# Kernel optimization log

Hardware: AMD Instinct MI355X
Metric: run time of the kernel (lower is better)

Reference implementation:

```python
import jax, jax.numpy as jnp
import numpy as np

COMMITMENT_COST = 0.25


def setup_inputs() -> dict:
    key = jax.random.key(0)
    k1, k2 = jax.random.split(key)
    z = jax.random.normal(k1, (32, 256, 32, 32), dtype=jnp.float32)
    # codebook init matches torch uniform_(-1/codebook_size, 1/codebook_size)
    embedding = jax.random.uniform(k2, (1024, 256), dtype=jnp.float32,
                                   minval=-1.0 / 1024, maxval=1.0 / 1024)
    return {"z": z, "embedding": embedding}


def reference(z, embedding):
    # z: [B, C, H, W] -> [B, H, W, C]
    z_bhwc = jnp.transpose(z.astype(jnp.float32), (0, 2, 3, 1))
    B, H, W, C = z_bhwc.shape
    z_flat = z_bhwc.reshape(-1, C)                      # [N, C]

    # squared-distance matrix via norms + matmul: [N, K]
    d = (jnp.sum(z_flat ** 2, axis=1, keepdims=True)
         + jnp.sum(embedding ** 2, axis=1)
         - 2.0 * jnp.einsum('nc,kc->nk', z_flat, embedding))

    min_encoding_indices = jnp.argmin(d, axis=1)        # [N]
    z_quantized = embedding[min_encoding_indices].reshape(B, H, W, C)

    commitment_loss = COMMITMENT_COST * (jax.lax.stop_gradient(z_quantized) - z_bhwc) ** 2
    codebook_loss = (z_quantized - jax.lax.stop_gradient(z_bhwc)) ** 2
    loss = commitment_loss + codebook_loss              # [B, H, W, C]

    # straight-through estimator
    z_quantized = z_bhwc + jax.lax.stop_gradient(z_quantized - z_bhwc)
    z_quantized = jnp.transpose(z_quantized, (0, 3, 1, 2))  # [B, C, H, W]
    return z_quantized, loss, min_encoding_indices
```

## Files before the change

### kernel.cpp

```cpp
#include <hip/hip_runtime.h>

#define ZC     256
#define KCODES 1024
#define MARGIN 4e-4f
#define WIN    1e-4f
#define NPT    32768

typedef __attribute__((ext_vector_type(4))) float f32x4;
typedef __attribute__((ext_vector_type(8))) short s16x8;
typedef unsigned int u32t;
typedef u32t __attribute__((address_space(1))) as1_u32;
typedef u32t __attribute__((address_space(3))) as3_u32;

__device__ __forceinline__ void glds16(const void* g, void* l) {
    __builtin_amdgcn_global_load_lds((const as1_u32*)g, (as3_u32*)l, 16, 0, 0);
}
__device__ __forceinline__ unsigned short bf16_rn(float x) {
    union { float f; u32t u; } v; v.f = x;
    return (unsigned short)((v.u + 0x7FFFu + ((v.u >> 16) & 1u)) >> 16);
}

__global__ __launch_bounds__(256)
void vq_prep_z(const float* __restrict__ z, unsigned short* __restrict__ Ab)
{
    const int t = threadIdx.x, blk = blockIdx.x;
    const int pt = (blk >> 3) * 64 + (t & 63);
    const int c0 = (blk & 7) * 32 + (t >> 6) * 8;
    const int b = pt >> 10, hw = pt & 1023;
    const float* zp = z + (size_t)b * (ZC * 1024) + (size_t)c0 * 1024 + hw;

    unsigned short hi[8];
    #pragma unroll
    for (int j = 0; j < 8; ++j) hi[j] = bf16_rn(zp[(size_t)j * 1024]);
    uint4 ph;
    ph.x = (u32t)hi[0] | ((u32t)hi[1] << 16); ph.y = (u32t)hi[2] | ((u32t)hi[3] << 16);
    ph.z = (u32t)hi[4] | ((u32t)hi[5] << 16); ph.w = (u32t)hi[6] | ((u32t)hi[7] << 16);

    const size_t kb = (size_t)(c0 >> 6);
    const int sw = (c0 & 63) ^ ((pt & 7) << 3);
    *reinterpret_cast<uint4*>(Ab + kb * (32768ull * 64) + (size_t)pt * 64 + sw) = ph;
}

__global__ __launch_bounds__(256)
void vq_prep_e(const float* __restrict__ emb, unsigned short* __restrict__ Bb)
{
    const int t = threadIdx.x, blk = blockIdx.x;
    const int code = (blk >> 3) * 64 + (t & 63);
    const int c0 = (blk & 7) * 32 + (t >> 6) * 8;
    const float* ep = emb + (size_t)code * ZC + c0;

    unsigned short hi[8];
    #pragma unroll
    for (int j = 0; j < 8; ++j) hi[j] = bf16_rn(ep[j]);
    uint4 ph;
    ph.x = (u32t)hi[0] | ((u32t)hi[1] << 16); ph.y = (u32t)hi[2] | ((u32t)hi[3] << 16);
    ph.z = (u32t)hi[4] | ((u32t)hi[5] << 16); ph.w = (u32t)hi[6] | ((u32t)hi[7] << 16);

    const size_t kb = (size_t)(c0 >> 6);
    const int sw = (c0 & 63) ^ ((code & 7) << 3);
    *reinterpret_cast<uint4*>(Bb + kb * (1024ull * 64) + (size_t)code * 64 + sw) = ph;
}

__global__ __launch_bounds__(256)
void vq_ens_np(const float* __restrict__ emb, float* __restrict__ ens_np,
               int* __restrict__ cnt)
{
    if (blockIdx.x == 0 && threadIdx.x == 0) *cnt = 0;
    const int t = threadIdx.x, g = t >> 3, r = t & 7;
    const int code = blockIdx.x * 32 + g;
    const float* er = emb + (size_t)code * ZC;

    float lo, hi;
    {
        const float a0 = er[r], a1 = er[128 + r];
        lo = __fmul_rn(a0, a0); hi = __fmul_rn(a1, a1);
    }
    #pragma unroll
    for (int i = 1; i < 16; ++i) {
        const int c = 8 * i + r;
        const float a0 = er[c], a1 = er[128 + c];
        lo = __fadd_rn(lo, __fmul_rn(a0, a0));
        hi = __fadd_rn(hi, __fmul_rn(a1, a1));
    }
    #pragma unroll
    for (int mk = 1; mk < 8; mk <<= 1) {
        lo = __fadd_rn(lo, __shfl_xor(lo, mk));
        hi = __fadd_rn(hi, __shfl_xor(hi, mk));
    }
    if (r == 0) ens_np[code] = __fadd_rn(lo, hi);
}

__global__ __launch_bounds__(256, 2)
void vq_gemm_argmin(const unsigned short* __restrict__ Ab,
                    const unsigned short* __restrict__ Bb,
                    const float* __restrict__ ens_g,
                    float* __restrict__ partV1, float* __restrict__ partV2,
                    int* __restrict__ partI)
{
    __shared__ unsigned short As[64 * 64];
    __shared__ unsigned short Bs[128 * 64];

    const int t = threadIdx.x;
    const int lane = t & 63, wv = t >> 6;
    const int col = lane & 15, kg = lane >> 4;
    const int blk = blockIdx.x;
    const int pt0 = (blk >> 1) * 64;
    const int half = blk & 1;
    const int kx = (col & 7) << 3;

    int aoff[4][2], boff[2][2];
    #pragma unroll
    for (int m = 0; m < 4; ++m)
        #pragma unroll
        for (int s = 0; s < 2; ++s)
            aoff[m][s] = (m * 16 + col) * 64 + ((s * 32 + kg * 8) ^ kx);
    #pragma unroll
    for (int n = 0; n < 2; ++n)
        #pragma unroll
        for (int s = 0; s < 2; ++s)
            boff[n][s] = (wv * 32 + n * 16 + col) * 64 + ((s * 32 + kg * 8) ^ kx);

    f32x4 acc[4][2];
    #pragma unroll
    for (int m = 0; m < 4; ++m)
        #pragma unroll
        for (int n = 0; n < 2; ++n) acc[m][n] = (f32x4){0.f, 0.f, 0.f, 0.f};

    float v1[16], v2[16]; int id1[16];
    #pragma unroll
    for (int i = 0; i < 16; ++i) { v1[i] = 3.4e38f; v2[i] = 3.4e38f; id1[i] = 0; }

    for (int ci = 0; ci < 4; ++ci) {
        const int ct = half * 4 + ci;
        for (int ks = 0; ks < 4; ++ks) {
            const char* aS = (const char*)(Ab + (size_t)ks * 2097152ull + (size_t)pt0 * 64);
            const char* bS = (const char*)(Bb + (size_t)ks * 65536ull + (size_t)ct * 8192);

            __syncthreads();
            glds16(aS + t * 16,        (char*)As + t * 16);
            glds16(aS + 4096 + t * 16, (char*)As + 4096 + t * 16);
            #pragma unroll
            for (int q = 0; q < 4; ++q)
                glds16(bS + q * 4096 + t * 16, (char*)Bs + q * 4096 + t * 16);
            __syncthreads();

            s16x8 af[4][2], bf[2][2];
            #pragma unroll
            for (int m = 0; m < 4; ++m)
                #pragma unroll
                for (int s = 0; s < 2; ++s)
                    af[m][s] = *reinterpret_cast<const s16x8*>(As + aoff[m][s]);
            #pragma unroll
            for (int n = 0; n < 2; ++n)
                #pragma unroll
                for (int s = 0; s < 2; ++s)
                    bf[n][s] = *reinterpret_cast<const s16x8*>(Bs + boff[n][s]);
            #pragma unroll
            for (int m = 0; m < 4; ++m)
                #pragma unroll
                for (int n = 0; n < 2; ++n) {
                    acc[m][n] = __builtin_amdgcn_mfma_f32_16x16x32_bf16(af[m][0], bf[n][0], acc[m][n], 0, 0, 0);
                    acc[m][n] = __builtin_amdgcn_mfma_f32_16x16x32_bf16(af[m][1], bf[n][1], acc[m][n], 0, 0, 0);
                }

            if (ks == 3) {
                #pragma unroll
                for (int n = 0; n < 2; ++n) {
                    const int code = ct * 128 + wv * 32 + n * 16 + col;
                    const float en = ens_g[code];
                    #pragma unroll
                    for (int m = 0; m < 4; ++m)
                        #pragma unroll
                        for (int j = 0; j < 4; ++j) {
                            const float sc = fmaf(-2.f, acc[m][n][j], en);
                            const int sl = m * 4 + j;
                            if (sc < v1[sl]) { v2[sl] = v1[sl]; v1[sl] = sc; id1[sl] = code; }
                            else if (sc < v2[sl]) { v2[sl] = sc; }
                            acc[m][n][j] = 0.f;
                        }
                }
            }
        }
    }

    float w1[16], w2[16]; int wid[16];
    #pragma unroll
    for (int sl = 0; sl < 16; ++sl) {
        float a1 = v1[sl]; int ai = id1[sl]; float a2 = v2[sl];
        #pragma unroll
        for (int mk = 1; mk < 16; mk <<= 1) {
            const float o1 = __shfl_xor(a1, mk);
            const int   oi = __shfl_xor(ai, mk);
            const float o2 = __shfl_xor(a2, mk);
            if (o1 < a1)      { a2 = fminf(a1, o2); a1 = o1; ai = oi; }
            else if (o1 > a1) { a2 = fminf(a2, o1); }
            else              { a2 = (oi != ai) ? a1 : fminf(a2, o2); ai = (oi < ai) ? oi : ai; }
        }
        w1[sl] = a1; w2[sl] = a2; wid[sl] = ai;
    }

    __syncthreads();
    float* mv1 = reinterpret_cast<float*>(As);
    float* mv2 = mv1 + 256;
    int*   mid = reinterpret_cast<int*>(mv2 + 256);
    if (col == 0) {
        #pragma unroll
        for (int sl = 0; sl < 16; ++sl) {
            const int m = sl >> 2, j = sl & 3;
            const int p = m * 16 + kg * 4 + j;
            mv1[wv * 64 + p] = w1[sl];
            mv2[wv * 64 + p] = w2[sl];
            mid[wv * 64 + p] = wid[sl];
        }
    }
    __syncthreads();
    if (t < 64) {
        float a1 = mv1[t], a2 = mv2[t]; int ai = mid[t];
        #pragma unroll
        for (int w = 1; w < 4; ++w) {
            const float b1 = mv1[w * 64 + t], b2 = mv2[w * 64 + t];
            const int   bi = mid[w * 64 + t];
            if (b1 < a1)      { a2 = fminf(a1, b2); a1 = b1; ai = bi; }
            else if (b1 > a1) { a2 = fminf(a2, b1); }
            else              { a2 = a1; ai = (bi < ai) ? bi : ai; }
        }
        const int g = half * NPT + pt0 + t;
        partV1[g] = a1; partV2[g] = a2; partI[g] = ai;
    }
}

__global__ __launch_bounds__(256)
void vq_merge(const float* __restrict__ partV1, const float* __restrict__ partV2,
              const int* __restrict__ partI, float* __restrict__ out_idx)
{
    const int n = blockIdx.x * 256 + threadIdx.x;
    const float a1 = partV1[n],       a2 = partV2[n];
    const int   ai = partI[n];
    const float b1 = partV1[NPT + n], b2 = partV2[NPT + n];
    const int   bi = partI[NPT + n];
    float v1f, v2f; int idf;
    if (b1 < a1)      { v1f = b1; idf = bi; v2f = fminf(a1, b2); }
    else if (b1 > a1) { v1f = a1; idf = ai; v2f = fminf(a2, b1); }
    else              { v1f = a1; idf = (bi < ai) ? bi : ai; v2f = a1; }
    out_idx[n] = ((v2f - v1f) <= MARGIN) ? (-1.0f - (float)idf) : (float)idf;
}

__global__ __launch_bounds__(256)
void vq_compact(const float* __restrict__ idxf, int* __restrict__ cnt,
                int* __restrict__ list)
{
    const int n = blockIdx.x * 256 + threadIdx.x;
    if (idxf[n] < 0.f) { const int p = atomicAdd(cnt, 1); list[p] = n; }
}

__global__ __launch_bounds__(256, 1)
void vq_fixup6(const float* __restrict__ z, const float* __restrict__ emb,
               const float* __restrict__ ens_np, float* __restrict__ idxf,
               const int* __restrict__ cnt, const int* __restrict__ list)
{
    __shared__ float  zsb[4 * 264];
    __shared__ float  scr[4 * 1024];
    __shared__ float  znv[4];
    __shared__ float  smin[4];
    __shared__ int    pn[4];
    __shared__ float  redm[4];
    __shared__ int    candk[128];
    __shared__ int    candp[128];
    __shared__ int    ccnt;
    __shared__ double dred[4];
    __shared__ float  bestd_s[4];
    __shared__ int    bestk_s[4];

    const int t = threadIdx.x;
    const int g = t >> 3, r = t & 7;
    const int C = *cnt;
    const int base = blockIdx.x * 4;
    if (base >= C) return;
    const int npts = (C - base < 4) ? (C - base) : 4;

    if (t < 4) pn[t] = (base + t < C) ? list[base + t] : list[base];
    if (t == 0) ccnt = 0;
    __syncthreads();
    #pragma unroll
    for (int p = 0; p < 4; ++p) {
        const int n = pn[p];
        const int b = n >> 10, q = n & 1023;
        zsb[p * 264 + t] = z[(size_t)b * (ZC * 1024) + (size_t)t * 1024 + q];
    }
    __syncthreads();

    if (t < 32) {
        const float* zp = zsb + g * 264;
        float lo = __fmul_rn(zp[r], zp[r]);
        float hi = __fmul_rn(zp[128 + r], zp[128 + r]);
        #pragma unroll
        for (int i = 1; i < 16; ++i) {
            const int c = 8 * i + r;
            lo = __fadd_rn(lo, __fmul_rn(zp[c], zp[c]));
            hi = __fadd_rn(hi, __fmul_rn(zp[128 + c], zp[128 + c]));
        }
        #pragma unroll
        for (int mk = 1; mk < 8; mk <<= 1) {
            lo = __fadd_rn(lo, __shfl_xor(lo, mk));
            hi = __fadd_rn(hi, __shfl_xor(hi, mk));
        }
        if (r == 0) znv[g] = __fadd_rn(lo, hi);
    }

    const float* zb0 = zsb + 0 * 264 + r * 4;
    const float* zb1 = zsb + 1 * 264 + r * 4;
    const float* zb2 = zsb + 2 * 264 + r * 4;
    const float* zb3 = zsb + 3 * 264 + r * 4;

    float4 eA0, eA1, eA2, eA3, eA4, eA5, eA6, eA7;
    {
        const float* er = emb + (size_t)g * ZC + r * 4;
        eA0 = *reinterpret_cast<const float4*>(er);
        eA1 = *reinterpret_cast<const float4*>(er + 32);
        eA2 = *reinterpret_cast<const float4*>(er + 64);
        eA3 = *reinterpret_cast<const float4*>(er + 96);
        eA4 = *reinterpret_cast<const float4*>(er + 128);
        eA5 = *reinterpret_cast<const float4*>(er + 160);
        eA6 = *reinterpret_cast<const float4*>(er + 192);
        eA7 = *reinterpret_cast<const float4*>(er + 224);
    }

    for (int tile = 0; tile < 32; ++tile) {
        float4 eB0, eB1, eB2, eB3, eB4, eB5, eB6, eB7;
        if (tile < 31) {
            const float* er = emb + (size_t)(tile + 1) * 32 * ZC + (size_t)g * ZC + r * 4;
            eB0 = *reinterpret_cast<const float4*>(er);
            eB1 = *reinterpret_cast<const float4*>(er + 32);
            eB2 = *reinterpret_cast<const float4*>(er + 64);
            eB3 = *reinterpret_cast<const float4*>(er + 96);
            eB4 = *reinterpret_cast<const float4*>(er + 128);
            eB5 = *reinterpret_cast<const float4*>(er + 160);
            eB6 = *reinterpret_cast<const float4*>(er + 192);
            eB7 = *reinterpret_cast<const float4*>(er + 224);
        }

        float s0 = 0.f, s1 = 0.f, s2 = 0.f, s3 = 0.f;
        #define SCREEN_STEP(EV, OFF)                                           \
        {                                                                      \
            const float4 a0 = *reinterpret_cast<const float4*>(zb0 + (OFF));   \
            const float4 a1 = *reinterpret_cast<const float4*>(zb1 + (OFF));   \
            const float4 a2 = *reinterpret_cast<const float4*>(zb2 + (OFF));   \
            const float4 a3 = *reinterpret_cast<const float4*>(zb3 + (OFF));   \
            s0 = fmaf(EV.x, a0.x, s0); s0 = fmaf(EV.y, a0.y, s0);              \
            s0 = fmaf(EV.z, a0.z, s0); s0 = fmaf(EV.w, a0.w, s0);              \
            s1 = fmaf(EV.x, a1.x, s1); s1 = fmaf(EV.y, a1.y, s1);              \
            s1 = fmaf(EV.z, a1.z, s1); s1 = fmaf(EV.w, a1.w, s1);              \
            s2 = fmaf(EV.x, a2.x, s2); s2 = fmaf(EV.y, a2.y, s2);              \
            s2 = fmaf(EV.z, a2.z, s2); s2 = fmaf(EV.w, a2.w, s2);              \
            s3 = fmaf(EV.x, a3.x, s3); s3 = fmaf(EV.y, a3.y, s3);              \
            s3 = fmaf(EV.z, a3.z, s3); s3 = fmaf(EV.w, a3.w, s3);              \
        }
        SCREEN_STEP(eA0, 0)
        SCREEN_STEP(eA1, 32)
        SCREEN_STEP(eA2, 64)
        SCREEN_STEP(eA3, 96)
        SCREEN_STEP(eA4, 128)
        SCREEN_STEP(eA5, 160)
        SCREEN_STEP(eA6, 192)
        SCREEN_STEP(eA7, 224)
        #undef SCREEN_STEP

        #pragma unroll
        for (int mk = 1; mk < 8; mk <<= 1) {
            s0 += __shfl_xor(s0, mk);
            s1 += __shfl_xor(s1, mk);
            s2 += __shfl_xor(s2, mk);
            s3 += __shfl_xor(s3, mk);
        }
        if (r == 0) {
            const int code = tile * 32 + g;
            const float en = ens_np[code];
            scr[0 * 1024 + code] = fmaf(-2.f, s0, en);
            scr[1 * 1024 + code] = fmaf(-2.f, s1, en);
            scr[2 * 1024 + code] = fmaf(-2.f, s2, en);
            scr[3 * 1024 + code] = fmaf(-2.f, s3, en);
        }

        eA0 = eB0; eA1 = eB1; eA2 = eB2; eA3 = eB3;
        eA4 = eB4; eA5 = eB5; eA6 = eB6; eA7 = eB7;
    }
    __syncthreads();

    for (int p = 0; p < 4; ++p) {
        float m = fminf(fminf(scr[p * 1024 + t],       scr[p * 1024 + t + 256]),
                        fminf(scr[p * 1024 + t + 512], scr[p * 1024 + t + 768]));
        #pragma unroll
        for (int mk = 1; mk < 64; mk <<= 1) m = fminf(m, __shfl_xor(m, mk));
        if ((t & 63) == 0) redm[t >> 6] = m;
        __syncthreads();
        if (t == 0) smin[p] = fminf(fminf(redm[0], redm[1]), fminf(redm[2], redm[3]));
        __syncthreads();
    }

    for (int p = 0; p < 4; ++p) {
        #pragma unroll
        for (int rep = 0; rep < 4; ++rep) {
            const int code = rep * 256 + t;
            if (scr[p * 1024 + code] <= smin[p] + WIN) {
                const int pos = atomicAdd(&ccnt, 1);
                if (pos < 128) { candk[pos] = code; candp[pos] = p; }
            }
        }
    }
    __syncthreads();
    const int NC = (ccnt < 128) ? ccnt : 128;

    if (t < 4) { bestd_s[t] = 3.4e38f; bestk_s[t] = 0x7fffffff; }
    __syncthreads();
    for (int ci = 0; ci < NC; ++ci) {
        const int code = candk[ci], p = candp[ci];
        double dd = (double)emb[(size_t)code * ZC + t] * (double)zsb[p * 264 + t];
        #pragma unroll
        for (int mk = 1; mk < 64; mk <<= 1) dd = dd + __shfl_xor(dd, mk);
        if ((t & 63) == 0) dred[t >> 6] = dd;
        __syncthreads();
        if (t == 0) {
            const double tot = (dred[0] + dred[1]) + (dred[2] + dred[3]);
            const float t2f = (float)tot;
            const float d = __fsub_rn(__fadd_rn(znv[p], ens_np[code]),
                                      __fmul_rn(2.0f, t2f));
            if (d < bestd_s[p] || (d == bestd_s[p] && code < bestk_s[p])) {
                bestd_s[p] = d; bestk_s[p] = code;
            }
        }
        __syncthreads();
    }
    if (t < npts) idxf[pn[t]] = (float)bestk_s[t];
}

__global__ __launch_bounds__(256)
void vq_outputs_kernel(const float* __restrict__ z, const float* __restrict__ emb,
                       const float* __restrict__ idxf,
                       float* __restrict__ out_q, float* __restrict__ out_loss)
{
    __shared__ float zts[32 * 257];
    __shared__ int   ids[32];

    const int t  = threadIdx.x;
    const int bh = blockIdx.x;
    const int b  = bh >> 5, h = bh & 31;
    const int n0 = bh * 32;

    if (t < 32) ids[t] = (int)idxf[n0 + t];
    __syncthreads();

    const size_t zbase = (size_t)b * (ZC * 1024) + h * 32;

    for (int rep = 0; rep < 32; ++rep) {
        const int flat = rep * 256 + t;
        const int c = flat >> 5;
        const int ww = flat & 31;
        const size_t ga = zbase + (size_t)c * 1024 + ww;
        const float zv = z[ga];
        zts[ww * 257 + c] = zv;
        out_q[ga] = emb[(size_t)ids[ww] * ZC + c];
    }
    __syncthreads();

    for (int rep = 0; rep < 32; ++rep) {
        const float e = emb[(size_t)ids[rep] * ZC + t];
        const float d = e - zts[rep * 257 + t];
        out_loss[(size_t)(n0 + rep) * ZC + t] = 1.25f * d * d;
    }
}

extern "C" void kernel_launch(void* const* d_in, const int* in_sizes, int n_in,
                              void* d_out, int out_size, void* d_ws, size_t ws_size,
                              hipStream_t stream)
{
    const float* z   = (const float*)d_in[0];
    const float* emb = (const float*)d_in[1];
    float* out      = (float*)d_out;
    float* out_q    = out;
    float* out_loss = out + 8388608;
    float* out_idx  = out + 16777216;

    unsigned short* Ab = (unsigned short*)d_out;
    unsigned short* Bb = (unsigned short*)((char*)d_out + 33554432);
    float* ensg = (float*)((char*)d_out + 34603008);
    int*   cnt  = (int*)  ((char*)d_out + 34607104);
    int*   list = (int*)  ((char*)d_out + 34607168);
    float* pV1  = (float*)((char*)d_out + 34738240);
    float* pV2  = (float*)((char*)d_out + 35000384);
    int*   pI   = (int*)  ((char*)d_out + 35262528);

    vq_prep_z        <<<4096, 256, 0, stream>>>(z, Ab);
    vq_prep_e        <<<128,  256, 0, stream>>>(emb, Bb);
    vq_ens_np        <<<32,   256, 0, stream>>>(emb, ensg, cnt);
    vq_gemm_argmin   <<<1024, 256, 0, stream>>>(Ab, Bb, ensg, pV1, pV2, pI);
    vq_merge         <<<128,  256, 0, stream>>>(pV1, pV2, pI, out_idx);
    vq_compact       <<<128,  256, 0, stream>>>(out_idx, cnt, list);
    vq_fixup6        <<<8192, 256, 0, stream>>>(z, emb, ensg, out_idx, cnt, list);
    vq_outputs_kernel<<<1024, 256, 0, stream>>>(z, emb, out_idx, out_q, out_loss);
}
```

Baseline: 196.8 us.

## Reduce argmin candidates per code tile into shared memory and fuse compaction into merge

The GEMM kernel no longer keeps 16 per-row top-2 register arrays across all code tiles. After each 128-code tile it does a cross-lane shuffle reduction and folds the result into shared-memory top-2 slots, which cuts register pressure and may raise occupancy. The price is shuffle reductions on every tile instead of once at the end, plus shared-memory read-modify-write traffic. Separately, the compaction kernel is merged into the merge kernel, removing one launch and one re-read of the index array.

```diff
diff --git a/kernel.cpp b/kernel.cpp
--- a/kernel.cpp
+++ b/kernel.cpp
@@ -99,6 +99,9 @@
 {
     __shared__ unsigned short As[64 * 64];
     __shared__ unsigned short Bs[128 * 64];
+    __shared__ float sv1[4 * 64];
+    __shared__ float sv2[4 * 64];
+    __shared__ int   sid[4 * 64];
 
     const int t = threadIdx.x;
     const int lane = t & 63, wv = t >> 6;
@@ -126,9 +129,9 @@
         #pragma unroll
         for (int n = 0; n < 2; ++n) acc[m][n] = (f32x4){0.f, 0.f, 0.f, 0.f};
 
-    float v1[16], v2[16]; int id1[16];
-    #pragma unroll
-    for (int i = 0; i < 16; ++i) { v1[i] = 3.4e38f; v2[i] = 3.4e38f; id1[i] = 0; }
+    sv1[wv * 64 + lane] = 3.4e38f;
+    sv2[wv * 64 + lane] = 3.4e38f;
+    sid[wv * 64 + lane] = 0x7fffffff;
 
     for (int ci = 0; ci < 4; ++ci) {
         const int ct = half * 4 + ci;
@@ -162,64 +165,52 @@
                     acc[m][n] = __builtin_amdgcn_mfma_f32_16x16x32_bf16(af[m][0], bf[n][0], acc[m][n], 0, 0, 0);
                     acc[m][n] = __builtin_amdgcn_mfma_f32_16x16x32_bf16(af[m][1], bf[n][1], acc[m][n], 0, 0, 0);
                 }
-
-            if (ks == 3) {
+        }
+
+        {
+            const int code0 = ct * 128 + wv * 32 + col;
+            const int code1 = code0 + 16;
+            const float en0 = ens_g[code0];
+            const float en1 = ens_g[code1];
+            #pragma unroll
+            for (int m = 0; m < 4; ++m)
                 #pragma unroll
-                for (int n = 0; n < 2; ++n) {
-                    const int code = ct * 128 + wv * 32 + n * 16 + col;
-                    const float en = ens_g[code];
+                for (int j = 0; j < 4; ++j) {
+                    const float sc0 = fmaf(-2.f, acc[m][0][j], en0);
+                    const float sc1 = fmaf(-2.f, acc[m][1][j], en1);
+                    acc[m][0][j] = 0.f; acc[m][1][j] = 0.f;
+                    float a1, a2; int ai;
+                    if (sc0 <= sc1) { a1 = sc0; ai = code0; a2 = sc1; }
+                    else            { a1 = sc1; ai = code1; a2 = sc0; }
                     #pragma unroll
-                    for (int m = 0; m < 4; ++m)
-                        #pragma unroll
-                        for (int j = 0; j < 4; ++j) {
-                            const float sc = fmaf(-2.f, acc[m][n][j], en);
-                            const int sl = m * 4 + j;
-                            if (sc < v1[sl]) { v2[sl] = v1[sl]; v1[sl] = sc; id1[sl] = code; }
-                            else if (sc < v2[sl]) { v2[sl] = sc; }
-                            acc[m][n][j] = 0.f;
+                    for (int mk = 1; mk < 16; mk <<= 1) {
+                        const float o1 = __shfl_xor(a1, mk);
+                        const int   oi = __shfl_xor(ai, mk);
+                        const float o2 = __shfl_xor(a2, mk);
+                        if (o1 < a1)      { a2 = fminf(a1, o2); a1 = o1; ai = oi; }
+                        else if (o1 > a1) { a2 = fminf(a2, o1); }
+                        else              { a2 = (oi != ai) ? a1 : fminf(a2, o2); ai = (oi < ai) ? oi : ai; }
+                    }
+                    if (col == 0) {
+                        const int idx = wv * 64 + m * 16 + kg * 4 + j;
+                        const float o1 = sv1[idx], o2 = sv2[idx];
+                        if (a1 < o1) {
+                            sv1[idx] = a1; sid[idx] = ai; sv2[idx] = fminf(o1, a2);
+                        } else {
+                            sv2[idx] = fminf(o2, a1);
                         }
+                    }
                 }
-            }
-        }
-    }
-
-    float w1[16], w2[16]; int wid[16];
-    #pragma unroll
-    for (int sl = 0; sl < 16; ++sl) {
-        float a1 = v1[sl]; int ai = id1[sl]; float a2 = v2[sl];
-        #pragma unroll
-        for (int mk = 1; mk < 16; mk <<= 1) {
-            const float o1 = __shfl_xor(a1, mk);
-            const int   oi = __shfl_xor(ai, mk);
-            const float o2 = __shfl_xor(a2, mk);
-            if (o1 < a1)      { a2 = fminf(a1, o2); a1 = o1; ai = oi; }
-            else if (o1 > a1) { a2 = fminf(a2, o1); }
-            else              { a2 = (oi != ai) ? a1 : fminf(a2, o2); ai = (oi < ai) ? oi : ai; }
-        }
-        w1[sl] = a1; w2[sl] = a2; wid[sl] = ai;
-    }
-
-    __syncthreads();
-    float* mv1 = reinterpret_cast<float*>(As);
-    float* mv2 = mv1 + 256;
-    int*   mid = reinterpret_cast<int*>(mv2 + 256);
-    if (col == 0) {
-        #pragma unroll
-        for (int sl = 0; sl < 16; ++sl) {
-            const int m = sl >> 2, j = sl & 3;
-            const int p = m * 16 + kg * 4 + j;
-            mv1[wv * 64 + p] = w1[sl];
-            mv2[wv * 64 + p] = w2[sl];
-            mid[wv * 64 + p] = wid[sl];
-        }
-    }
+        }
+    }
+
     __syncthreads();
     if (t < 64) {
-        float a1 = mv1[t], a2 = mv2[t]; int ai = mid[t];
+        float a1 = sv1[t], a2 = sv2[t]; int ai = sid[t];
         #pragma unroll
         for (int w = 1; w < 4; ++w) {
-            const float b1 = mv1[w * 64 + t], b2 = mv2[w * 64 + t];
-            const int   bi = mid[w * 64 + t];
+            const float b1 = sv1[w * 64 + t], b2 = sv2[w * 64 + t];
+            const int   bi = sid[w * 64 + t];
             if (b1 < a1)      { a2 = fminf(a1, b2); a1 = b1; ai = bi; }
             else if (b1 > a1) { a2 = fminf(a2, b1); }
             else              { a2 = a1; ai = (bi < ai) ? bi : ai; }
@@ -231,7 +222,8 @@
 
 __global__ __launch_bounds__(256)
 void vq_merge(const float* __restrict__ partV1, const float* __restrict__ partV2,
-              const int* __restrict__ partI, float* __restrict__ out_idx)
+              const int* __restrict__ partI, float* __restrict__ out_idx,
+              int* __restrict__ cnt, int* __restrict__ list)
 {
     const int n = blockIdx.x * 256 + threadIdx.x;
     const float a1 = partV1[n],       a2 = partV2[n];
@@ -242,15 +234,9 @@
     if (b1 < a1)      { v1f = b1; idf = bi; v2f = fminf(a1, b2); }
     else if (b1 > a1) { v1f = a1; idf = ai; v2f = fminf(a2, b1); }
     else              { v1f = a1; idf = (bi < ai) ? bi : ai; v2f = a1; }
-    out_idx[n] = ((v2f - v1f) <= MARGIN) ? (-1.0f - (float)idf) : (float)idf;
-}
-
-__global__ __launch_bounds__(256)
-void vq_compact(const float* __restrict__ idxf, int* __restrict__ cnt,
-                int* __restrict__ list)
-{
-    const int n = blockIdx.x * 256 + threadIdx.x;
-    if (idxf[n] < 0.f) { const int p = atomicAdd(cnt, 1); list[p] = n; }
+    const bool flag = (v2f - v1f) <= MARGIN;
+    out_idx[n] = flag ? (-1.0f - (float)idf) : (float)idf;
+    if (flag) { const int pos = atomicAdd(cnt, 1); list[pos] = n; }
 }
 
 __global__ __launch_bounds__(256, 1)
@@ -493,8 +479,7 @@
     vq_prep_e        <<<128,  256, 0, stream>>>(emb, Bb);
     vq_ens_np        <<<32,   256, 0, stream>>>(emb, ensg, cnt);
     vq_gemm_argmin   <<<1024, 256, 0, stream>>>(Ab, Bb, ensg, pV1, pV2, pI);
-    vq_merge         <<<128,  256, 0, stream>>>(pV1, pV2, pI, out_idx);
-    vq_compact       <<<128,  256, 0, stream>>>(out_idx, cnt, list);
+    vq_merge         <<<128,  256, 0, stream>>>(pV1, pV2, pI, out_idx, cnt, list);
     vq_fixup6        <<<8192, 256, 0, stream>>>(z, emb, ensg, out_idx, cnt, list);
     vq_outputs_kernel<<<1024, 256, 0, stream>>>(z, emb, out_idx, out_q, out_loss);
 }
```

New measurement: 183.1 us, median of 2. -7.0%, faster.
